# Kernel optimization log

Hardware: AMD Instinct MI355X
Metric: run time of the kernel (lower is better)

## Reference

```python
import jax, jax.numpy as jnp
import numpy as np

BS = 2
EMBED = 256
NH = 8
NL = 4
NP = 4
HD = EMBED // NH
SHAPES = [(128, 128), (64, 64), (32, 32), (16, 16)]
NQ = sum(h * w for h, w in SHAPES)  # 21760


def setup_inputs() -> dict:
    key = jax.random.key(0)
    ks = jax.random.split(key, 12)
    s = 1.0 / np.sqrt(EMBED)
    return {
        "query": jax.random.normal(ks[0], (BS, NQ, EMBED), jnp.float32),
        "reference_points": jax.random.uniform(ks[1], (BS, NQ, NL, 2), jnp.float32),
        "value": jax.random.normal(ks[2], (BS, NQ, EMBED), jnp.float32),
        "W_off": jax.random.normal(ks[3], (EMBED, NH * NL * NP * 2), jnp.float32) * 0.01,
        "b_off": jax.random.normal(ks[4], (NH * NL * NP * 2,), jnp.float32) * 0.5,
        "W_attn": jax.random.normal(ks[5], (EMBED, NH * NL * NP), jnp.float32) * 0.02,
        "b_attn": jnp.zeros((NH * NL * NP,), jnp.float32),
        "W_v": jax.random.normal(ks[6], (EMBED, EMBED), jnp.float32) * s,
        "b_v": jnp.zeros((EMBED,), jnp.float32),
        "W_out": jax.random.normal(ks[7], (EMBED, EMBED), jnp.float32) * s,
        "b_out": jnp.zeros((EMBED,), jnp.float32),
        "value_spatial_shapes": np.asarray(SHAPES, dtype=np.int64),
    }


def _ms_deform_attn(value, shapes, loc, aw):
    # value: [bs,V,nh,d]; loc: [bs,nq,nh,L,P,2] in [0,1]; aw: [bs,nq,nh,L,P]
    bs, V, nh, d = value.shape
    nq = loc.shape[1]
    out = jnp.zeros((bs, nq, nh, d), value.dtype)
    start = 0
    b_idx = jnp.arange(bs)[:, None, None, None]
    h_idx = jnp.arange(nh)[None, None, :, None]
    for l, (H, W) in enumerate(shapes):
        H, W = int(H), int(W)
        v = value[:, start:start + H * W].reshape(bs, H, W, nh, d)
        start += H * W
        g = 2.0 * loc[:, :, :, l] - 1.0  # [bs,nq,nh,P,2], grid_sample convention
        # align_corners=False pixel coordinates
        x = ((g[..., 0] + 1.0) * W - 1.0) * 0.5
        y = ((g[..., 1] + 1.0) * H - 1.0) * 0.5
        x0 = jnp.floor(x); y0 = jnp.floor(y)
        wx1 = x - x0; wx0 = 1.0 - wx1
        wy1 = y - y0; wy0 = 1.0 - wy1

        def gather(yi, xi):
            inb = (yi >= 0) & (yi < H) & (xi >= 0) & (xi < W)
            yc = jnp.clip(yi, 0, H - 1).astype(jnp.int32)
            xc = jnp.clip(xi, 0, W - 1).astype(jnp.int32)
            vals = v[b_idx, yc, xc, h_idx]  # [bs,nq,nh,P,d]
            return vals * inb[..., None].astype(v.dtype)

        samp = (gather(y0, x0) * (wy0 * wx0)[..., None]
                + gather(y0, x0 + 1) * (wy0 * wx1)[..., None]
                + gather(y0 + 1, x0) * (wy1 * wx0)[..., None]
                + gather(y0 + 1, x0 + 1) * (wy1 * wx1)[..., None])
        out = out + jnp.einsum('bqhpd,bqhp->bqhd', samp, aw[:, :, :, l])
    return out.reshape(bs, nq, nh * d)


def reference(query, reference_points, value, W_off, b_off, W_attn, b_attn,
              W_v, b_v, W_out, b_out, value_spatial_shapes):
    shapes = np.asarray(value_spatial_shapes)  # static [L,2]
    bs, nq, _ = query.shape
    v = (value @ W_v + b_v).reshape(bs, -1, NH, HD)
    off = (query @ W_off + b_off).reshape(bs, nq, NH, NL, NP, 2)
    aw = (query @ W_attn + b_attn).reshape(bs, nq, NH, NL * NP)
    aw = jax.nn.softmax(aw, axis=-1).reshape(bs, nq, NH, NL, NP)
    # offset normalizer: (W,H) per level
    norm = jnp.asarray(shapes[:, ::-1].astype(np.float32))  # [L,2]
    loc = reference_points[:, :, None, :, None, :] + off / norm[None, None, None, :, None, :]
    out = _ms_deform_attn(v, shapes, loc, aw)
    return out @ W_out + b_out
```

## Files before the change

### kernel.cpp

```cpp
#include <hip/hip_runtime.h>
#include <math.h>

#define BS 2
#define NQ 21760
#define V_LEN 21760
#define EMBED 256
#define NH 8
#define NL 4
#define NP 4
#define HD 32

typedef __bf16 bf16;
typedef __bf16 bf16x8 __attribute__((ext_vector_type(8)));
typedef __bf16 bf16x4 __attribute__((ext_vector_type(4)));
typedef float f32x4 __attribute__((ext_vector_type(4)));
typedef float f32x2 __attribute__((ext_vector_type(2)));
typedef unsigned int u32;

#define GLOAD_LDS16(gp, lp_) \
    __builtin_amdgcn_global_load_lds( \
        (const __attribute__((address_space(1))) unsigned int*)(gp), \
        (__attribute__((address_space(3))) unsigned int*)(lp_), 16, 0, 0)

__global__ __launch_bounds__(256) void cast_all(
    const float* __restrict__ W_v, const float* __restrict__ W_off,
    const float* __restrict__ W_attn, const float* __restrict__ W_out,
    const float* __restrict__ b_off, const float* __restrict__ b_attn,
    bf16* __restrict__ WTv, bf16* __restrict__ WToa, bf16* __restrict__ WTu,
    float* __restrict__ bcat)
{
    const int bid = blockIdx.x;
    const int tid = threadIdx.x;
    if (bid == 56) {
        if (tid < 384) bcat[tid] = (tid < 256) ? b_off[tid] : b_attn[tid - 256];
        return;
    }
    const float* W; bf16* WT; int N, tile;
    if (bid < 16)      { W = W_v;    WT = WTv;           N = 256; tile = bid; }
    else if (bid < 32) { W = W_off;  WT = WToa;          N = 256; tile = bid - 16; }
    else if (bid < 40) { W = W_attn; WT = WToa + 65536;  N = 128; tile = bid - 32; }
    else               { W = W_out;  WT = WTu;           N = 256; tile = bid - 40; }
    const int ntn = N >> 6;
    const int k0 = (tile / ntn) * 64, n0 = (tile % ntn) * 64;

    __shared__ float lds[64][65];
    const int c = tid & 63, r4 = tid >> 6;
    #pragma unroll
    for (int p = 0; p < 16; p++) {
        int rr = r4 + p * 4;
        lds[rr][c] = W[(size_t)(k0 + rr) * N + n0 + c];
    }
    __syncthreads();
    #pragma unroll
    for (int p = 0; p < 16; p++) {
        int i = r4 + p * 4;
        WT[(size_t)(n0 + i) * 256 + k0 + c] = (bf16)lds[c][i];
    }
}

template<bool A_F32, int OUT_MODE>
__global__ __launch_bounds__(256) void gemm_mfma(
    const void* __restrict__ Av, const bf16* __restrict__ WT,
    const float* __restrict__ bias, void* __restrict__ Cv,
    int N, int K, int ntn)
{
    const int nmt = gridDim.x / ntn;
    const int bmt = blockIdx.x % nmt;
    const int bnt = blockIdx.x / nmt;
    const int bm = bmt * 128, bn = bnt * 128;

    __shared__ __align__(16) bf16 Bs[2][128 * 32];
    __shared__ __align__(16) unsigned char AsRaw[2][A_F32 ? 128 * 32 * 4
                                                         : 128 * 32 * 2];

    const int tid = threadIdx.x;
    const int lane = tid & 63, wv = tid >> 6;
    const int wr = wv >> 1, wc = wv & 1;
    const int quad = lane >> 4, l16 = lane & 15;

    f32x4 acc[4][4];
    #pragma unroll
    for (int i = 0; i < 4; i++)
        #pragma unroll
        for (int j = 0; j < 4; j++)
            acc[i][j] = (f32x4){0.f, 0.f, 0.f, 0.f};

    const int b_row = tid >> 2, b_chunk = tid & 3;
    const int a_row8 = tid >> 3, a_phys = tid & 7;
    constexpr int NB = A_F32 ? 6 : 4;

    auto stage = [&](int buf, int k0) {
        if constexpr (A_F32) {
            const float* A = (const float*)Av;
            #pragma unroll
            for (int p = 0; p < 4; p++) {
                int row = a_row8 + p * 32;
                int csrc = a_phys ^ (row & 7);
                GLOAD_LDS16(&A[(size_t)(bm + row) * K + k0 + csrc * 4],
                            &AsRaw[buf][p * 4096 + tid * 16]);
            }
        } else {
            const bf16* A = (const bf16*)Av;
            #pragma unroll
            for (int p = 0; p < 2; p++) {
                int row = b_row + p * 64;
                GLOAD_LDS16(&A[(size_t)(bm + row) * K + k0 + b_chunk * 8],
                            &AsRaw[buf][p * 4096 + tid * 16]);
            }
        }
        #pragma unroll
        for (int p = 0; p < 2; p++) {
            int row = b_row + p * 64;
            GLOAD_LDS16(&WT[(size_t)(bn + row) * K + k0 + b_chunk * 8],
                        (unsigned char*)&Bs[buf][0] + p * 4096 + tid * 16);
        }
    };

    const int nt = K >> 5;
    stage(0, 0);
    int cur = 0;
    for (int t = 0; t < nt; t++) {
        __builtin_amdgcn_s_barrier();
        if (t + 1 < nt) {
            stage(cur ^ 1, (t + 1) << 5);
            asm volatile("s_waitcnt vmcnt(%0)" :: "n"(NB) : "memory");
        } else {
            asm volatile("s_waitcnt vmcnt(0)" ::: "memory");
        }
        __builtin_amdgcn_s_barrier();

        bf16x8 af[4], bfr[4];
        if constexpr (A_F32) {
            const float* Asf = (const float*)&AsRaw[cur][0];
            #pragma unroll
            for (int mi = 0; mi < 4; mi++) {
                int r = wr * 64 + mi * 16 + l16;
                int g = r & 7;
                f32x4 u0 = *(const f32x4*)&Asf[r * 32 + ((2 * quad) ^ g) * 4];
                f32x4 u1 = *(const f32x4*)&Asf[r * 32 + ((2 * quad + 1) ^ g) * 4];
                bf16x8 hh;
                hh[0] = (bf16)u0[0]; hh[1] = (bf16)u0[1]; hh[2] = (bf16)u0[2]; hh[3] = (bf16)u0[3];
                hh[4] = (bf16)u1[0]; hh[5] = (bf16)u1[1]; hh[6] = (bf16)u1[2]; hh[7] = (bf16)u1[3];
                af[mi] = hh;
            }
        } else {
            const bf16* Asb = (const bf16*)&AsRaw[cur][0];
            #pragma unroll
            for (int mi = 0; mi < 4; mi++) {
                int r = wr * 64 + mi * 16 + l16;
                af[mi] = *(const bf16x8*)&Asb[r * 32 + quad * 8];
            }
        }
        #pragma unroll
        for (int ni = 0; ni < 4; ni++) {
            int r = wc * 64 + ni * 16 + l16;
            bfr[ni] = *(const bf16x8*)&Bs[cur][r * 32 + quad * 8];
        }
        #pragma unroll
        for (int mi = 0; mi < 4; mi++)
            #pragma unroll
            for (int ni = 0; ni < 4; ni++)
                acc[mi][ni] = __builtin_amdgcn_mfma_f32_16x16x32_bf16(
                    af[mi], bfr[ni], acc[mi][ni], 0, 0, 0);
        cur ^= 1;
    }

    #pragma unroll
    for (int mi = 0; mi < 4; mi++) {
        #pragma unroll
        for (int ni = 0; ni < 4; ni++) {
            const int col = bn + wc * 64 + ni * 16 + l16;
            const int row0 = bm + wr * 64 + mi * 16 + quad * 4;
            const float bc = bias[col];
            #pragma unroll
            for (int r = 0; r < 4; r++) {
                float v = acc[mi][ni][r] + bc;
                if constexpr (OUT_MODE == 0) {
                    ((float*)Cv)[(size_t)(row0 + r) * N + col] = v;
                } else if constexpr (OUT_MODE == 1) {
                    ((bf16*)Cv)[(size_t)(row0 + r) * N + col] = (bf16)v;
                } else {
                    int rv = row0 + r;
                    int bb = (rv >= V_LEN) ? 1 : 0;
                    int vv = rv - bb * V_LEN;
                    ((bf16*)Cv)[((size_t)(bb * NH + (col >> 5)) * V_LEN + vv) * 32
                                + (col & 31)] = (bf16)v;
                }
            }
        }
    }
}

__device__ inline void acc8(const uint4& rr, float ww,
                            f32x2& a01, f32x2& a23, f32x2& a45, f32x2& a67)
{
    f32x2 v;
    v[0] = __uint_as_float(rr.x << 16); v[1] = __uint_as_float(rr.x & 0xFFFF0000u); a01 += v * ww;
    v[0] = __uint_as_float(rr.y << 16); v[1] = __uint_as_float(rr.y & 0xFFFF0000u); a23 += v * ww;
    v[0] = __uint_as_float(rr.z << 16); v[1] = __uint_as_float(rr.z & 0xFFFF0000u); a45 += v * ww;
    v[0] = __uint_as_float(rr.w << 16); v[1] = __uint_as_float(rr.w & 0xFFFF0000u); a67 += v * ww;
}

__global__ __launch_bounds__(256) void deform_sample(
    const bf16* __restrict__ vproj, const float* __restrict__ offaw,
    const float* __restrict__ refp, bf16* __restrict__ sampled)
{
    const int wv = threadIdx.x >> 6;
    const int t = threadIdx.x & 63;
    const int q = blockIdx.x * 4 + wv;
    const int b = blockIdx.y;
    const int bq = b * NQ + q;

    __shared__ __align__(16) float s_w[4][128][4];
    __shared__ __align__(16) int   s_idx[4][128];

    const float* row = offaw + (size_t)bq * 384;

    const int hp = t & 7, e = t >> 3;
    float l0 = row[256 + hp * 16 + e];
    float l1 = row[256 + hp * 16 + e + 8];
    float m = fmaxf(l0, l1);
    m = fmaxf(m, __shfl_xor(m, 8));
    m = fmaxf(m, __shfl_xor(m, 16));
    m = fmaxf(m, __shfl_xor(m, 32));
    float e0 = __expf(l0 - m), e1 = __expf(l1 - m);
    float ssum = e0 + e1;
    ssum += __shfl_xor(ssum, 8);
    ssum += __shfl_xor(ssum, 16);
    ssum += __shfl_xor(ssum, 32);
    float rs = 1.0f / ssum;
    float awv[2] = {e0 * rs, e1 * rs};

    #pragma unroll
    for (int sI = 0; sI < 2; sI++) {
        int lp = e + sI * 8;
        int l = lp >> 2;
        int Wl = 128 >> l, Hl = 128 >> l;
        int st = (l == 0) ? 0 : (l == 1) ? 16384 : (l == 2) ? 20480 : 21504;
        float2 rp = *(const float2*)&refp[((size_t)bq * 4 + l) * 2];
        float2 oxy = *(const float2*)&row[hp * 32 + lp * 2];
        float fW = (float)Wl, fH = (float)Hl;
        float x = (rp.x + oxy.x / fW) * fW - 0.5f;
        float y = (rp.y + oxy.y / fH) * fH - 0.5f;
        float xf = floorf(x), yf = floorf(y);
        int x0 = (int)xf, y0 = (int)yf;
        float wx1 = x - xf, wx0 = 1.f - wx1;
        float wy1 = y - yf, wy0 = 1.f - wy1;
        float aw = awv[sI];
        float wx0p = ((x0 >= 0) && (x0 < Wl)) ? wx0 : 0.f;
        float wx1p = ((x0 + 1 >= 0) && (x0 + 1 < Wl)) ? wx1 : 0.f;
        float wy0p = ((y0 >= 0) && (y0 < Hl)) ? wy0 : 0.f;
        float wy1p = ((y0 + 1 >= 0) && (y0 + 1 < Hl)) ? wy1 : 0.f;
        int px = min(max(x0, 0), Wl - 2), py = min(max(y0, 0), Hl - 2);
        int cx0 = min(max(x0, 0), Wl - 1), cx1 = min(max(x0 + 1, 0), Wl - 1);
        int cy0 = min(max(y0, 0), Hl - 1), cy1 = min(max(y0 + 1, 0), Hl - 1);
        float sx0 = ((cx0 == px) ? wx0p : 0.f) + ((cx1 == px) ? wx1p : 0.f);
        float sx1 = ((cx0 == px + 1) ? wx0p : 0.f) + ((cx1 == px + 1) ? wx1p : 0.f);
        float sy0 = ((cy0 == py) ? wy0p : 0.f) + ((cy1 == py) ? wy1p : 0.f);
        float sy1 = ((cy0 == py + 1) ? wy0p : 0.f) + ((cy1 == py + 1) ? wy1p : 0.f);
        int d = lp * 8 + hp;
        s_idx[wv][d] = st + py * Wl + px;
        s_w[wv][d][0] = sy0 * sx0 * aw;
        s_w[wv][d][1] = sy0 * sx1 * aw;
        s_w[wv][d][2] = sy1 * sx0 * aw;
        s_w[wv][d][3] = sy1 * sx1 * aw;
    }
    __syncthreads();

    const int h = t >> 3, j = t & 7;
    const bf16* vb = vproj + ((size_t)(b * NH + h) * V_LEN) * 32 + j * 8;

    f32x2 a01 = {0.f, 0.f}, a23 = {0.f, 0.f}, a45 = {0.f, 0.f}, a67 = {0.f, 0.f};
    #pragma unroll
    for (int lp = 0; lp < 16; lp++) {
        const int Wl = 128 >> (lp >> 2);
        const int d = lp * 8 + h;
        const int base = s_idx[wv][d];
        const float4 w4 = *(const float4*)&s_w[wv][d][0];
        const bf16* p0 = vb + (size_t)base * 32;
        uint4 r0 = *(const uint4*)p0;
        uint4 r1 = *(const uint4*)(p0 + Wl * 32);
        const bool xs = (j & 4) != 0;
        float wA = xs ? w4.y : w4.x;
        float wB = xs ? w4.w : w4.z;
        acc8(r0, wA, a01, a23, a45, a67);
        acc8(r1, wB, a01, a23, a45, a67);
    }

    float s[8] = {a01[0], a01[1], a23[0], a23[1], a45[0], a45[1], a67[0], a67[1]};
    #pragma unroll
    for (int i = 0; i < 8; i++) s[i] += __shfl_xor(s[i], 4);

    if ((t & 4) == 0) {
        bf16x8 o;
        #pragma unroll
        for (int i = 0; i < 8; i++) o[i] = (bf16)s[i];
        *(bf16x8*)&sampled[(size_t)bq * 256 + h * 32 + (t & 3) * 8] = o;
    }
}

extern "C" void kernel_launch(void* const* d_in, const int* in_sizes, int n_in,
                              void* d_out, int out_size, void* d_ws, size_t ws_size,
                              hipStream_t stream)
{
    const float* query  = (const float*)d_in[0];
    const float* refp   = (const float*)d_in[1];
    const float* value  = (const float*)d_in[2];
    const float* W_off  = (const float*)d_in[3];
    const float* b_off  = (const float*)d_in[4];
    const float* W_attn = (const float*)d_in[5];
    const float* b_attn = (const float*)d_in[6];
    const float* W_v    = (const float*)d_in[7];
    const float* b_v    = (const float*)d_in[8];
    const float* W_out  = (const float*)d_in[9];
    const float* b_out  = (const float*)d_in[10];
    float* out = (float*)d_out;

    const int M = BS * NQ;

    char* ws = (char*)d_ws;
    bf16*  WTv   = (bf16*)ws;                      ws += 256 * 256 * 2;
    bf16*  WToa  = (bf16*)ws;                      ws += 384 * 256 * 2;
    bf16*  WTu   = (bf16*)ws;                      ws += 256 * 256 * 2;
    float* bcat  = (float*)ws;                     ws += 384 * 4;
    bf16*  vproj = (bf16*)ws;                      ws += (size_t)M * 256 * 2;
    float* offaw = (float*)ws;                     ws += (size_t)M * 384 * 4;
    bf16*  samp  = (bf16*)ws;                      ws += (size_t)M * 256 * 2;

    cast_all<<<57, 256, 0, stream>>>(W_v, W_off, W_attn, W_out, b_off, b_attn,
                                     WTv, WToa, WTu, bcat);

    gemm_mfma<true, 2><<<(M / 128) * 2, 256, 0, stream>>>(value, WTv, b_v, vproj, 256, 256, 2);
    gemm_mfma<true, 0><<<(M / 128) * 3, 256, 0, stream>>>(query, WToa, bcat, offaw, 384, 256, 3);
    deform_sample<<<dim3(NQ / 4, BS), dim3(256), 0, stream>>>(vproj, offaw, refp, samp);
    gemm_mfma<false, 0><<<(M / 128) * 2, 256, 0, stream>>>(samp, WTu, b_out, out, 256, 256, 2);
}
```

Baseline: 283.5 us.

## Fuse output projection into deform sampling and merge input GEMMs into one launch

The value and offset/attention projections now run in a single dual GEMM launch, with block index selecting the problem. The output projection is folded into the sampling kernel. Each 1024-thread block samples 16 queries into LDS, then each wave computes 16 output columns with MFMA, reading W_out directly from global memory. This removes the bf16 sampled intermediate round trip and one launch. In exchange, blocks are larger and use more LDS, which may reduce occupancy, and W_out is re-read per block.

```diff
diff --git a/kernel.cpp b/kernel.cpp
--- a/kernel.cpp
+++ b/kernel.cpp
@@ -58,20 +58,30 @@
     }
 }
 
-template<bool A_F32, int OUT_MODE>
-__global__ __launch_bounds__(256) void gemm_mfma(
-    const void* __restrict__ Av, const bf16* __restrict__ WT,
-    const float* __restrict__ bias, void* __restrict__ Cv,
-    int N, int K, int ntn)
-{
-    const int nmt = gridDim.x / ntn;
-    const int bmt = blockIdx.x % nmt;
-    const int bnt = blockIdx.x / nmt;
+__global__ __launch_bounds__(256) void gemm_dual(
+    const float* __restrict__ A1, const bf16* __restrict__ WT1,
+    const float* __restrict__ bias1, void* __restrict__ C1,
+    const float* __restrict__ A2, const bf16* __restrict__ WT2,
+    const float* __restrict__ bias2, void* __restrict__ C2,
+    int nblk1)
+{
+    const float* A; const bf16* WT; const float* bias; void* Cv;
+    int N, ntn, bidx, mode;
+    if ((int)blockIdx.x < nblk1) {
+        A = A1; WT = WT1; bias = bias1; Cv = C1; N = 256; ntn = 2;
+        bidx = blockIdx.x; mode = 1;
+    } else {
+        A = A2; WT = WT2; bias = bias2; Cv = C2; N = 384; ntn = 3;
+        bidx = blockIdx.x - nblk1; mode = 0;
+    }
+    const int nmt = (BS * NQ) / 128;
+    const int bmt = bidx % nmt;
+    const int bnt = bidx / nmt;
     const int bm = bmt * 128, bn = bnt * 128;
+    const int K = 256;
 
     __shared__ __align__(16) bf16 Bs[2][128 * 32];
-    __shared__ __align__(16) unsigned char AsRaw[2][A_F32 ? 128 * 32 * 4
-                                                         : 128 * 32 * 2];
+    __shared__ __align__(16) float Asf[2][128 * 32];
 
     const int tid = threadIdx.x;
     const int lane = tid & 63, wv = tid >> 6;
@@ -87,26 +97,15 @@
 
     const int b_row = tid >> 2, b_chunk = tid & 3;
     const int a_row8 = tid >> 3, a_phys = tid & 7;
-    constexpr int NB = A_F32 ? 6 : 4;
+    constexpr int NB = 6;
 
     auto stage = [&](int buf, int k0) {
-        if constexpr (A_F32) {
-            const float* A = (const float*)Av;
-            #pragma unroll
-            for (int p = 0; p < 4; p++) {
-                int row = a_row8 + p * 32;
-                int csrc = a_phys ^ (row & 7);
-                GLOAD_LDS16(&A[(size_t)(bm + row) * K + k0 + csrc * 4],
-                            &AsRaw[buf][p * 4096 + tid * 16]);
-            }
-        } else {
-            const bf16* A = (const bf16*)Av;
-            #pragma unroll
-            for (int p = 0; p < 2; p++) {
-                int row = b_row + p * 64;
-                GLOAD_LDS16(&A[(size_t)(bm + row) * K + k0 + b_chunk * 8],
-                            &AsRaw[buf][p * 4096 + tid * 16]);
-            }
+        #pragma unroll
+        for (int p = 0; p < 4; p++) {
+            int row = a_row8 + p * 32;
+            int csrc = a_phys ^ (row & 7);
+            GLOAD_LDS16(&A[(size_t)(bm + row) * K + k0 + csrc * 4],
+                        (unsigned char*)&Asf[buf][0] + p * 4096 + tid * 16);
         }
         #pragma unroll
         for (int p = 0; p < 2; p++) {
@@ -116,12 +115,11 @@
         }
     };
 
-    const int nt = K >> 5;
     stage(0, 0);
     int cur = 0;
-    for (int t = 0; t < nt; t++) {
+    for (int t = 0; t < 8; t++) {
         __builtin_amdgcn_s_barrier();
-        if (t + 1 < nt) {
+        if (t + 1 < 8) {
             stage(cur ^ 1, (t + 1) << 5);
             asm volatile("s_waitcnt vmcnt(%0)" :: "n"(NB) : "memory");
         } else {
@@ -130,26 +128,16 @@
         __builtin_amdgcn_s_barrier();
 
         bf16x8 af[4], bfr[4];
-        if constexpr (A_F32) {
-            const float* Asf = (const float*)&AsRaw[cur][0];
-            #pragma unroll
-            for (int mi = 0; mi < 4; mi++) {
-                int r = wr * 64 + mi * 16 + l16;
-                int g = r & 7;
-                f32x4 u0 = *(const f32x4*)&Asf[r * 32 + ((2 * quad) ^ g) * 4];
-                f32x4 u1 = *(const f32x4*)&Asf[r * 32 + ((2 * quad + 1) ^ g) * 4];
-                bf16x8 hh;
-                hh[0] = (bf16)u0[0]; hh[1] = (bf16)u0[1]; hh[2] = (bf16)u0[2]; hh[3] = (bf16)u0[3];
-                hh[4] = (bf16)u1[0]; hh[5] = (bf16)u1[1]; hh[6] = (bf16)u1[2]; hh[7] = (bf16)u1[3];
-                af[mi] = hh;
-            }
-        } else {
-            const bf16* Asb = (const bf16*)&AsRaw[cur][0];
-            #pragma unroll
-            for (int mi = 0; mi < 4; mi++) {
-                int r = wr * 64 + mi * 16 + l16;
-                af[mi] = *(const bf16x8*)&Asb[r * 32 + quad * 8];
-            }
+        #pragma unroll
+        for (int mi = 0; mi < 4; mi++) {
+            int r = wr * 64 + mi * 16 + l16;
+            int g = r & 7;
+            f32x4 u0 = *(const f32x4*)&Asf[cur][r * 32 + ((2 * quad) ^ g) * 4];
+            f32x4 u1 = *(const f32x4*)&Asf[cur][r * 32 + ((2 * quad + 1) ^ g) * 4];
+            bf16x8 hh;
+            hh[0] = (bf16)u0[0]; hh[1] = (bf16)u0[1]; hh[2] = (bf16)u0[2]; hh[3] = (bf16)u0[3];
+            hh[4] = (bf16)u1[0]; hh[5] = (bf16)u1[1]; hh[6] = (bf16)u1[2]; hh[7] = (bf16)u1[3];
+            af[mi] = hh;
         }
         #pragma unroll
         for (int ni = 0; ni < 4; ni++) {
@@ -175,15 +163,13 @@
             #pragma unroll
             for (int r = 0; r < 4; r++) {
                 float v = acc[mi][ni][r] + bc;
-                if constexpr (OUT_MODE == 0) {
+                if (mode == 0) {
                     ((float*)Cv)[(size_t)(row0 + r) * N + col] = v;
-                } else if constexpr (OUT_MODE == 1) {
-                    ((bf16*)Cv)[(size_t)(row0 + r) * N + col] = (bf16)v;
                 } else {
                     int rv = row0 + r;
-                    int bb = (rv >= V_LEN) ? 1 : 0;
-                    int vv = rv - bb * V_LEN;
-                    ((bf16*)Cv)[((size_t)(bb * NH + (col >> 5)) * V_LEN + vv) * 32
+                    int bb2 = (rv >= V_LEN) ? 1 : 0;
+                    int vv = rv - bb2 * V_LEN;
+                    ((bf16*)Cv)[((size_t)(bb2 * NH + (col >> 5)) * V_LEN + vv) * 32
                                 + (col & 31)] = (bf16)v;
                 }
             }
@@ -201,18 +187,20 @@
     v[0] = __uint_as_float(rr.w << 16); v[1] = __uint_as_float(rr.w & 0xFFFF0000u); a67 += v * ww;
 }
 
-__global__ __launch_bounds__(256) void deform_sample(
+__global__ __launch_bounds__(1024, 4) void deform_out(
     const bf16* __restrict__ vproj, const float* __restrict__ offaw,
-    const float* __restrict__ refp, bf16* __restrict__ sampled)
+    const float* __restrict__ refp, const bf16* __restrict__ WTu,
+    const float* __restrict__ b_out, float* __restrict__ out)
 {
     const int wv = threadIdx.x >> 6;
     const int t = threadIdx.x & 63;
-    const int q = blockIdx.x * 4 + wv;
     const int b = blockIdx.y;
-    const int bq = b * NQ + q;
-
-    __shared__ __align__(16) float s_w[4][128][4];
-    __shared__ __align__(16) int   s_idx[4][128];
+    const int q0 = blockIdx.x * 16;
+    const int bq = b * NQ + q0 + wv;
+
+    __shared__ __align__(16) float s_w[16][128][4];
+    __shared__ __align__(16) int   s_idx[16][128];
+    __shared__ __align__(16) bf16  s_samp[16][264];
 
     const float* row = offaw + (size_t)bq * 384;
 
@@ -265,7 +253,6 @@
         s_w[wv][d][2] = sy1 * sx0 * aw;
         s_w[wv][d][3] = sy1 * sx1 * aw;
     }
-    __syncthreads();
 
     const int h = t >> 3, j = t & 7;
     const bf16* vb = vproj + ((size_t)(b * NH + h) * V_LEN) * 32 + j * 8;
@@ -295,8 +282,24 @@
         bf16x8 o;
         #pragma unroll
         for (int i = 0; i < 8; i++) o[i] = (bf16)s[i];
-        *(bf16x8*)&sampled[(size_t)bq * 256 + h * 32 + (t & 3) * 8] = o;
-    }
+        *(bf16x8*)&s_samp[wv][h * 32 + (t & 3) * 8] = o;
+    }
+    __syncthreads();
+
+    const int quad = t >> 4, l16 = t & 15;
+    const int col = wv * 16 + l16;
+    const bf16* wrow = WTu + (size_t)col * 256;
+    f32x4 oacc = (f32x4){0.f, 0.f, 0.f, 0.f};
+    #pragma unroll
+    for (int ks = 0; ks < 8; ks++) {
+        bf16x8 afr = *(const bf16x8*)&s_samp[l16][ks * 32 + quad * 8];
+        bf16x8 bfr = *(const bf16x8*)&wrow[ks * 32 + quad * 8];
+        oacc = __builtin_amdgcn_mfma_f32_16x16x32_bf16(afr, bfr, oacc, 0, 0, 0);
+    }
+    const float bc = b_out[col];
+    #pragma unroll
+    for (int r = 0; r < 4; r++)
+        out[(size_t)(b * NQ + q0 + quad * 4 + r) * 256 + col] = oacc[r] + bc;
 }
 
 extern "C" void kernel_launch(void* const* d_in, const int* in_sizes, int n_in,
@@ -325,13 +328,15 @@
     float* bcat  = (float*)ws;                     ws += 384 * 4;
     bf16*  vproj = (bf16*)ws;                      ws += (size_t)M * 256 * 2;
     float* offaw = (float*)ws;                     ws += (size_t)M * 384 * 4;
-    bf16*  samp  = (bf16*)ws;                      ws += (size_t)M * 256 * 2;
 
     cast_all<<<57, 256, 0, stream>>>(W_v, W_off, W_attn, W_out, b_off, b_attn,
                                      WTv, WToa, WTu, bcat);
 
-    gemm_mfma<true, 2><<<(M / 128) * 2, 256, 0, stream>>>(value, WTv, b_v, vproj, 256, 256, 2);
-    gemm_mfma<true, 0><<<(M / 128) * 3, 256, 0, stream>>>(query, WToa, bcat, offaw, 384, 256, 3);
-    deform_sample<<<dim3(NQ / 4, BS), dim3(256), 0, stream>>>(vproj, offaw, refp, samp);
-    gemm_mfma<false, 0><<<(M / 128) * 2, 256, 0, stream>>>(samp, WTu, b_out, out, 256, 256, 2);
-}
+    const int nblk1 = (M / 128) * 2;
+    gemm_dual<<<nblk1 + (M / 128) * 3, 256, 0, stream>>>(
+        value, WTv, b_v, vproj,
+        query, WToa, bcat, offaw, nblk1);
+
+    deform_out<<<dim3(NQ / 16, BS), dim3(1024), 0, stream>>>(
+        vproj, offaw, refp, WTu, b_out, out);
+}
```

Measured after the change: 301.6 us. +6.4%, slower.

## Remap deformable sampling to per-head blocks with one corner load per thread

Applied to the files above, without the earlier changes.

Restructures the sampling kernel so each block handles one (batch, head) pair for 16 queries. Each 16-lane group computes the 16 softmax weights and sample coordinates for one query-head. Each lane then gathers a single 16-byte corner slice per sample, instead of two rows for one x-slot across all heads. The block-wide barrier is dropped because each wave reads only the shared-memory entries it wrote itself. In exchange the offset/logit rows and reference points are re-read by eight different blocks, and the output needs an extra shuffle-reduction stage.

```diff
diff --git a/kernel.cpp b/kernel.cpp
--- a/kernel.cpp
+++ b/kernel.cpp
@@ -201,44 +201,50 @@
     v[0] = __uint_as_float(rr.w << 16); v[1] = __uint_as_float(rr.w & 0xFFFF0000u); a67 += v * ww;
 }
 
-__global__ __launch_bounds__(256) void deform_sample(
+__global__ __launch_bounds__(256) void deform_head(
     const bf16* __restrict__ vproj, const float* __restrict__ offaw,
     const float* __restrict__ refp, bf16* __restrict__ sampled)
 {
+    const int gid = blockIdx.x;
+    const int idx8 = gid & 7;
+    const int mid = gid >> 3;
+    const int qg = mid % (NQ / 16);
+    const int hsel = mid / (NQ / 16);
+    const int h = (idx8 >> 1) + (hsel << 2);
+    const int b = idx8 & 1;
+
     const int wv = threadIdx.x >> 6;
     const int t = threadIdx.x & 63;
-    const int q = blockIdx.x * 4 + wv;
-    const int b = blockIdx.y;
+    const int qq = t >> 4, s = t & 15;
+    const int q = qg * 16 + wv * 4 + qq;
     const int bq = b * NQ + q;
-
-    __shared__ __align__(16) float s_w[4][128][4];
-    __shared__ __align__(16) int   s_idx[4][128];
+    const int wq = wv * 4 + qq;
+
+    __shared__ __align__(16) float s_w[16][16][4];
+    __shared__ int s_idx[16][16];
 
     const float* row = offaw + (size_t)bq * 384;
 
-    const int hp = t & 7, e = t >> 3;
-    float l0 = row[256 + hp * 16 + e];
-    float l1 = row[256 + hp * 16 + e + 8];
-    float m = fmaxf(l0, l1);
+    float lg = row[256 + h * 16 + s];
+    float m = lg;
+    m = fmaxf(m, __shfl_xor(m, 1));
+    m = fmaxf(m, __shfl_xor(m, 2));
+    m = fmaxf(m, __shfl_xor(m, 4));
     m = fmaxf(m, __shfl_xor(m, 8));
-    m = fmaxf(m, __shfl_xor(m, 16));
-    m = fmaxf(m, __shfl_xor(m, 32));
-    float e0 = __expf(l0 - m), e1 = __expf(l1 - m);
-    float ssum = e0 + e1;
+    float ev = __expf(lg - m);
+    float ssum = ev;
+    ssum += __shfl_xor(ssum, 1);
+    ssum += __shfl_xor(ssum, 2);
+    ssum += __shfl_xor(ssum, 4);
     ssum += __shfl_xor(ssum, 8);
-    ssum += __shfl_xor(ssum, 16);
-    ssum += __shfl_xor(ssum, 32);
-    float rs = 1.0f / ssum;
-    float awv[2] = {e0 * rs, e1 * rs};
-
-    #pragma unroll
-    for (int sI = 0; sI < 2; sI++) {
-        int lp = e + sI * 8;
-        int l = lp >> 2;
-        int Wl = 128 >> l, Hl = 128 >> l;
+    float aw = ev * (1.0f / ssum);
+
+    {
+        int l = s >> 2;
+        int Wl = 128 >> l, Hl = Wl;
         int st = (l == 0) ? 0 : (l == 1) ? 16384 : (l == 2) ? 20480 : 21504;
         float2 rp = *(const float2*)&refp[((size_t)bq * 4 + l) * 2];
-        float2 oxy = *(const float2*)&row[hp * 32 + lp * 2];
+        float2 oxy = *(const float2*)&row[h * 32 + s * 2];
         float fW = (float)Wl, fH = (float)Hl;
         float x = (rp.x + oxy.x / fW) * fW - 0.5f;
         float y = (rp.y + oxy.y / fH) * fH - 0.5f;
@@ -246,7 +252,6 @@
         int x0 = (int)xf, y0 = (int)yf;
         float wx1 = x - xf, wx0 = 1.f - wx1;
         float wy1 = y - yf, wy0 = 1.f - wy1;
-        float aw = awv[sI];
         float wx0p = ((x0 >= 0) && (x0 < Wl)) ? wx0 : 0.f;
         float wx1p = ((x0 + 1 >= 0) && (x0 + 1 < Wl)) ? wx1 : 0.f;
         float wy0p = ((y0 >= 0) && (y0 < Hl)) ? wy0 : 0.f;
@@ -258,44 +263,42 @@
         float sx1 = ((cx0 == px + 1) ? wx0p : 0.f) + ((cx1 == px + 1) ? wx1p : 0.f);
         float sy0 = ((cy0 == py) ? wy0p : 0.f) + ((cy1 == py) ? wy1p : 0.f);
         float sy1 = ((cy0 == py + 1) ? wy0p : 0.f) + ((cy1 == py + 1) ? wy1p : 0.f);
-        int d = lp * 8 + hp;
-        s_idx[wv][d] = st + py * Wl + px;
-        s_w[wv][d][0] = sy0 * sx0 * aw;
-        s_w[wv][d][1] = sy0 * sx1 * aw;
-        s_w[wv][d][2] = sy1 * sx0 * aw;
-        s_w[wv][d][3] = sy1 * sx1 * aw;
-    }
-    __syncthreads();
-
-    const int h = t >> 3, j = t & 7;
-    const bf16* vb = vproj + ((size_t)(b * NH + h) * V_LEN) * 32 + j * 8;
+        s_idx[wq][s] = st + py * Wl + px;
+        s_w[wq][s][0] = sy0 * sx0 * aw;
+        s_w[wq][s][1] = sy0 * sx1 * aw;
+        s_w[wq][s][2] = sy1 * sx0 * aw;
+        s_w[wq][s][3] = sy1 * sx1 * aw;
+    }
+
+    const int chgrp = t & 3;
+    const int xslot = (t >> 2) & 1;
+    const int rowsel = (t >> 3) & 1;
+    const int widx = rowsel * 2 + xslot;
+    const bf16* vb = vproj + (size_t)(b * NH + h) * V_LEN * 32;
 
     f32x2 a01 = {0.f, 0.f}, a23 = {0.f, 0.f}, a45 = {0.f, 0.f}, a67 = {0.f, 0.f};
     #pragma unroll
-    for (int lp = 0; lp < 16; lp++) {
-        const int Wl = 128 >> (lp >> 2);
-        const int d = lp * 8 + h;
-        const int base = s_idx[wv][d];
-        const float4 w4 = *(const float4*)&s_w[wv][d][0];
-        const bf16* p0 = vb + (size_t)base * 32;
-        uint4 r0 = *(const uint4*)p0;
-        uint4 r1 = *(const uint4*)(p0 + Wl * 32);
-        const bool xs = (j & 4) != 0;
-        float wA = xs ? w4.y : w4.x;
-        float wB = xs ? w4.w : w4.z;
-        acc8(r0, wA, a01, a23, a45, a67);
-        acc8(r1, wB, a01, a23, a45, a67);
-    }
-
-    float s[8] = {a01[0], a01[1], a23[0], a23[1], a45[0], a45[1], a67[0], a67[1]};
-    #pragma unroll
-    for (int i = 0; i < 8; i++) s[i] += __shfl_xor(s[i], 4);
-
-    if ((t & 4) == 0) {
+    for (int i = 0; i < 16; i++) {
+        const int Wl = 128 >> (i >> 2);
+        int base = s_idx[wq][i];
+        float w = s_w[wq][i][widx];
+        const bf16* p = vb + (size_t)(base + rowsel * Wl + xslot) * 32 + chgrp * 8;
+        uint4 r = *(const uint4*)p;
+        acc8(r, w, a01, a23, a45, a67);
+    }
+
+    float sarr[8] = {a01[0], a01[1], a23[0], a23[1], a45[0], a45[1], a67[0], a67[1]};
+    #pragma unroll
+    for (int i = 0; i < 8; i++) {
+        sarr[i] += __shfl_xor(sarr[i], 4);
+        sarr[i] += __shfl_xor(sarr[i], 8);
+    }
+
+    if ((t & 12) == 0) {
         bf16x8 o;
         #pragma unroll
-        for (int i = 0; i < 8; i++) o[i] = (bf16)s[i];
-        *(bf16x8*)&sampled[(size_t)bq * 256 + h * 32 + (t & 3) * 8] = o;
+        for (int i = 0; i < 8; i++) o[i] = (bf16)sarr[i];
+        *(bf16x8*)&sampled[(size_t)bq * 256 + h * 32 + chgrp * 8] = o;
     }
 }
 
@@ -332,6 +335,6 @@
 
     gemm_mfma<true, 2><<<(M / 128) * 2, 256, 0, stream>>>(value, WTv, b_v, vproj, 256, 256, 2);
     gemm_mfma<true, 0><<<(M / 128) * 3, 256, 0, stream>>>(query, WToa, bcat, offaw, 384, 256, 3);
-    deform_sample<<<dim3(NQ / 4, BS), dim3(256), 0, stream>>>(vproj, offaw, refp, samp);
+    deform_head<<<2 * NH * (NQ / 16), 256, 0, stream>>>(vproj, offaw, refp, samp);
     gemm_mfma<false, 0><<<(M / 128) * 2, 256, 0, stream>>>(samp, WTu, b_out, out, 256, 256, 2);
 }
```

Measured after the change: 268.6 us. 1.06x faster.
